# Kernel optimization log

Hardware: AMD Instinct MI355X
Metric: run time of the kernel (lower is better)

The kernel has to match this reference:

```python
import jax, jax.numpy as jnp
import numpy as np

N = 50_000
E = 800_000
H = 128
EDGE_DIM = 1
NEG = 0.01  # leaky_relu slope used throughout AttentiveFP


def _lrelu(x):
    return jnp.where(x >= 0, x, NEG * x)


def _seg_softmax(logits, seg, num_segments):
    # numerically stable softmax over edges grouped by target segment
    m = jax.ops.segment_max(logits, seg, num_segments=num_segments)
    e = jnp.exp(logits - m[seg])
    s = jax.ops.segment_sum(e, seg, num_segments=num_segments)
    return e / s[seg]


def _gru(x, h, Wih, Whh, bih, bhh):
    # torch.nn.GRUCell: gates ordered r, z, n
    gi = x @ Wih.T + bih
    gh = h @ Whh.T + bhh
    ir, iz, inn = jnp.split(gi, 3, axis=-1)
    hr, hz, hn = jnp.split(gh, 3, axis=-1)
    r = jax.nn.sigmoid(ir + hr)
    z = jax.nn.sigmoid(iz + hz)
    n = jnp.tanh(inn + r * hn)
    return (1.0 - z) * n + z * h


def setup_inputs() -> dict:
    key = jax.random.key(0)
    ks = jax.random.split(key, 32)
    def rn(k, shape, s=0.1):
        return jax.random.normal(k, shape, dtype=jnp.float32) * s
    return {
        "node_attr": jax.random.normal(ks[0], (N, 1), dtype=jnp.float32),
        "edge_index": jax.random.randint(ks[1], (2, E), 0, N),
        "edge_attr": jax.random.normal(ks[2], (E, EDGE_DIM), dtype=jnp.float32),
        "W_lin1": rn(ks[3], (H, 1)), "b_lin1": rn(ks[4], (H,)),
        "gate_W1": rn(ks[5], (H, H + EDGE_DIM)), "gate_W2": rn(ks[6], (H, H)),
        "gate_att_l": rn(ks[7], (H,)), "gate_att_r": rn(ks[8], (H,)),
        "gate_b": rn(ks[9], (H,)),
        "gru1_Wih": rn(ks[10], (3 * H, H)), "gru1_Whh": rn(ks[11], (3 * H, H)),
        "gru1_bih": rn(ks[12], (3 * H,)), "gru1_bhh": rn(ks[13], (3 * H,)),
        "atom_W": rn(ks[14], (H, H)), "atom_att_src": rn(ks[15], (H,)),
        "atom_att_dst": rn(ks[16], (H,)), "atom_b": rn(ks[17], (H,)),
        "gru2_Wih": rn(ks[18], (3 * H, H)), "gru2_Whh": rn(ks[19], (3 * H, H)),
        "gru2_bih": rn(ks[20], (3 * H,)), "gru2_bhh": rn(ks[21], (3 * H,)),
        "mol_W": rn(ks[22], (H, H)), "mol_att_src": rn(ks[23], (H,)),
        "mol_att_dst": rn(ks[24], (H,)), "mol_b": rn(ks[25], (H,)),
        "grum_Wih": rn(ks[26], (3 * H, H)), "grum_Whh": rn(ks[27], (3 * H, H)),
        "grum_bih": rn(ks[28], (3 * H,)), "grum_bhh": rn(ks[29], (3 * H,)),
    }


def _forward(node_attr, edge_index, edge_attr, W_lin1, b_lin1, gate_W1, gate_W2,
             gate_att_l, gate_att_r, gate_b, gru1_Wih, gru1_Whh, gru1_bih, gru1_bhh,
             atom_W, atom_att_src, atom_att_dst, atom_b, gru2_Wih, gru2_Whh,
             gru2_bih, gru2_bhh, mol_W, mol_att_src, mol_att_dst, mol_b,
             grum_Wih, grum_Whh, grum_bih, grum_bhh):
    src, dst = edge_index[0], edge_index[1]  # j -> i (aggregate at dst)
    n = node_attr.shape[0]
    # lin1 + leaky_relu
    x = _lrelu(node_attr @ W_lin1.T + b_lin1)  # [N,H]
    # --- GATEConv (edge-featured attention) ---
    xj = _lrelu(jnp.concatenate([x[src], edge_attr], axis=-1) @ gate_W1.T)  # [E,H]
    alpha = _lrelu(xj @ gate_att_l + (x @ gate_att_r)[dst])  # [E]
    alpha = _seg_softmax(alpha, dst, n)
    h = jax.ops.segment_sum((x[src] @ gate_W2.T) * alpha[:, None], dst, num_segments=n) + gate_b
    h = jax.nn.elu(h)
    x = jax.nn.relu(_gru(h, x, gru1_Wih, gru1_Whh, gru1_bih, gru1_bhh))
    # --- GATConv layer (num_layers=2 -> one) ---
    xt = x @ atom_W.T  # [N,H]
    a = _lrelu((xt * atom_att_src).sum(-1)[src] + (xt * atom_att_dst).sum(-1)[dst])
    a = _seg_softmax(a, dst, n)
    h = jax.ops.segment_sum(xt[src] * a[:, None], dst, num_segments=n) + atom_b
    h = jax.nn.elu(h)
    x = jax.nn.relu(_gru(h, x, gru2_Wih, gru2_Whh, gru2_bih, gru2_bhh))
    # --- molecule embedding: batch = zeros -> single graph; num_timesteps=1 ---
    batch = jnp.zeros((n,), dtype=jnp.int32)
    out = jax.nn.relu(jax.ops.segment_sum(x, batch, num_segments=1))  # [1,H]
    xs = x @ mol_W.T          # node-side transform (shared lin)
    outs = out @ mol_W.T      # graph-side transform
    a = _lrelu((xs * mol_att_src).sum(-1) + (outs * mol_att_dst).sum(-1)[batch])
    a = _seg_softmax(a, batch, 1)
    h = jax.nn.elu(jax.ops.segment_sum(xs * a[:, None], batch, num_segments=1) + mol_b)
    out = jax.nn.relu(_gru(h, out, grum_Wih, grum_Whh, grum_bih, grum_bhh))
    return out  # [1, H] graph embedding (layer1 output, out_channels=hidden)


def reference(node_attr, edge_index, edge_attr, W_lin1, b_lin1, gate_W1, gate_W2,
              gate_att_l, gate_att_r, gate_b, gru1_Wih, gru1_Whh, gru1_bih, gru1_bhh,
              atom_W, atom_att_src, atom_att_dst, atom_b, gru2_Wih, gru2_Whh,
              gru2_bih, gru2_bhh, mol_W, mol_att_src, mol_att_dst, mol_b,
              grum_Wih, grum_Whh, grum_bih, grum_bhh):
    return _forward(node_attr, edge_index, edge_attr, W_lin1, b_lin1, gate_W1,
                    gate_W2, gate_att_l, gate_att_r, gate_b, gru1_Wih, gru1_Whh,
                    gru1_bih, gru1_bhh, atom_W, atom_att_src, atom_att_dst, atom_b,
                    gru2_Wih, gru2_Whh, gru2_bih, gru2_bhh, mol_W, mol_att_src,
                    mol_att_dst, mol_b, grum_Wih, grum_Whh, grum_bih, grum_bhh)
```

## Files before the change

kernel.cpp:

```cpp
#include <hip/hip_runtime.h>
#include <math.h>

#define H 128
#define NEGS 0.01f

typedef __attribute__((ext_vector_type(8))) short short8;
typedef __attribute__((ext_vector_type(4))) float f32x4;

__device__ __forceinline__ float lrelu(float x){ return x >= 0.f ? x : NEGS*x; }
__device__ __forceinline__ float eluf(float x){ return x > 0.f ? x : expf(x)-1.f; }
__device__ __forceinline__ float sigm(float x){ return 1.f/(1.f+expf(-x)); }
__device__ __forceinline__ float wred(float v){
  #pragma unroll
  for (int off = 32; off > 0; off >>= 1) v += __shfl_xor(v, off, 64);
  return v;
}
__device__ __forceinline__ float wredmax(float v){
  #pragma unroll
  for (int off = 32; off > 0; off >>= 1) v = fmaxf(v, __shfl_xor(v, off, 64));
  return v;
}
__device__ __forceinline__ unsigned fenc(float f){
  unsigned u = __float_as_uint(f);
  return (u & 0x80000000u) ? ~u : (u | 0x80000000u);
}
__device__ __forceinline__ float fdec(unsigned v){
  return __uint_as_float((v & 0x80000000u) ? (v ^ 0x80000000u) : ~v);
}
__device__ __forceinline__ unsigned short f2bf(float f){
  unsigned u = __float_as_uint(f);
  u += 0x7fffu + ((u >> 16) & 1u);
  return (unsigned short)(u >> 16);
}
__device__ __forceinline__ float bf2f(unsigned short h){
  return __uint_as_float(((unsigned)h) << 16);
}
__device__ __forceinline__ float rdlane(float v, int l){
  return __int_as_float(__builtin_amdgcn_readlane(__float_as_int(v), l));
}
__device__ __forceinline__ int rdlanei(int v, int l){
  return __builtin_amdgcn_readlane(v, l);
}

__global__ void k_castall(const float* __restrict__ gW1, const float* __restrict__ gW2,
                          const float* __restrict__ atomW, const float* __restrict__ molW,
                          const float* __restrict__ g1ih, const float* __restrict__ g1hh,
                          const float* __restrict__ g2ih, const float* __restrict__ g2hh,
                          unsigned short* __restrict__ dst){
  int idx = blockIdx.x*256 + threadIdx.x;
  const float* src; int ld = 128; int off;
  if      (idx <  16384){ src = gW1;  ld = 129; off = idx; }
  else if (idx <  32768){ src = gW2;  off = idx -  16384; }
  else if (idx <  49152){ src = atomW;off = idx -  32768; }
  else if (idx <  65536){ src = molW; off = idx -  49152; }
  else if (idx < 114688){ src = g1ih; off = idx -  65536; }
  else if (idx < 163840){ src = g1hh; off = idx - 114688; }
  else if (idx < 212992){ src = g2ih; off = idx - 163840; }
  else                  { src = g2hh; off = idx - 212992; }
  int r = off >> 7, c = off & 127;
  dst[idx] = f2bf(src[r*ld + c]);
}

__global__ void k_node_init_rd(const float* __restrict__ na, const float* __restrict__ wl,
                               const float* __restrict__ bl, const float* __restrict__ attr,
                               unsigned short* __restrict__ x, float* __restrict__ rdot, int n){
  int i = blockIdx.x*4 + (threadIdx.x >> 6);
  int lane = threadIdx.x & 63;
  if (i >= n) return;
  float nav = na[i];
  float v0 = lrelu(nav*wl[2*lane]   + bl[2*lane]);
  float v1 = lrelu(nav*wl[2*lane+1] + bl[2*lane+1]);
  ushort2 o; o.x = f2bf(v0); o.y = f2bf(v1);
  *(ushort2*)&x[(size_t)i*H + 2*lane] = o;
  float d = bf2f(o.x)*attr[2*lane] + bf2f(o.y)*attr[2*lane+1];
  d = wred(d);
  if (lane == 0) rdot[i] = d;
}

__global__ __launch_bounds__(256)
void k_gemm_mfma(const unsigned short* __restrict__ X, const unsigned short* __restrict__ Wbf,
                 unsigned short* __restrict__ Y, int n, int ldy,
                 const float* __restrict__ v1, const float* __restrict__ v2,
                 float* __restrict__ o1, float* __restrict__ o2){
  int w = threadIdx.x >> 6;
  int l = threadIdx.x & 63;
  int i0 = blockIdx.x*64 + w*16;
  int mbase = blockIdx.y*128;
  int row = l & 15;
  int kg  = l >> 4;
  f32x4 acc[8];
  #pragma unroll
  for (int c = 0; c < 8; ++c) acc[c] = (f32x4){0.f,0.f,0.f,0.f};
  int ai = i0 + row;
  bool av = (ai < n);
  #pragma unroll
  for (int ks = 0; ks < 4; ++ks){
    int koff = ks*32 + kg*8;
    short8 a = av ? *(const short8*)&X[(size_t)ai*H + koff]
                  : (short8){0,0,0,0,0,0,0,0};
    #pragma unroll
    for (int c = 0; c < 8; ++c){
      short8 b = *(const short8*)&Wbf[(size_t)(mbase + c*16 + row)*H + koff];
      acc[c] = __builtin_amdgcn_mfma_f32_16x16x32_bf16(a, b, acc[c], 0, 0, 0);
    }
  }
  #pragma unroll
  for (int c = 0; c < 8; ++c){
    #pragma unroll
    for (int r = 0; r < 4; ++r){
      int i = i0 + kg*4 + r;
      if (i < n) Y[(size_t)i*ldy + mbase + c*16 + row] = f2bf(acc[c][r]);
    }
  }
  if (v1){
    #pragma unroll
    for (int r = 0; r < 4; ++r){
      float p1 = 0.f, p2 = 0.f;
      #pragma unroll
      for (int c = 0; c < 8; ++c){
        float av1 = v1[c*16 + row];
        p1 += acc[c][r]*av1;
        if (v2) p2 += acc[c][r]*v2[c*16 + row];
      }
      #pragma unroll
      for (int off = 1; off < 16; off <<= 1){
        p1 += __shfl_xor(p1, off, 64);
        if (v2) p2 += __shfl_xor(p2, off, 64);
      }
      int i = i0 + kg*4 + r;
      if (row == 0 && i < n){ o1[i] = p1; if (v2) o2[i] = p2; }
    }
  }
}

__global__ void k_gru_combine(const unsigned short* __restrict__ gi, const unsigned short* __restrict__ gh,
                              const float* __restrict__ bih, const float* __restrict__ bhh,
                              unsigned short* __restrict__ x, int n){
  int idx = blockIdx.x*blockDim.x + threadIdx.x;
  if (idx >= n*64) return;
  int i = idx >> 6, t = (idx & 63)*2;
  const unsigned short* gir = gi + (size_t)i*384;
  const unsigned short* ghr = gh + (size_t)i*384;
  ushort2 uir = *(const ushort2*)&gir[t];
  ushort2 uiz = *(const ushort2*)&gir[t+128];
  ushort2 uin = *(const ushort2*)&gir[t+256];
  ushort2 uhr = *(const ushort2*)&ghr[t];
  ushort2 uhz = *(const ushort2*)&ghr[t+128];
  ushort2 uhn = *(const ushort2*)&ghr[t+256];
  ushort2 ux  = *(const ushort2*)&x[(size_t)i*H + t];
  float2 b_ir = *(const float2*)&bih[t], b_iz = *(const float2*)&bih[t+128], b_in = *(const float2*)&bih[t+256];
  float2 b_hr = *(const float2*)&bhh[t], b_hz = *(const float2*)&bhh[t+128], b_hn = *(const float2*)&bhh[t+256];
  ushort2 o;
  {
    float r = sigm(bf2f(uir.x)+b_ir.x + bf2f(uhr.x)+b_hr.x);
    float z = sigm(bf2f(uiz.x)+b_iz.x + bf2f(uhz.x)+b_hz.x);
    float nn = tanhf(bf2f(uin.x)+b_in.x + r*(bf2f(uhn.x)+b_hn.x));
    o.x = f2bf(fmaxf((1.f-z)*nn + z*bf2f(ux.x), 0.f));
  }
  {
    float r = sigm(bf2f(uir.y)+b_ir.y + bf2f(uhr.y)+b_hr.y);
    float z = sigm(bf2f(uiz.y)+b_iz.y + bf2f(uhz.y)+b_hz.y);
    float nn = tanhf(bf2f(uin.y)+b_in.y + r*(bf2f(uhn.y)+b_hn.y));
    o.y = f2bf(fmaxf((1.f-z)*nn + z*bf2f(ux.y), 0.f));
  }
  *(ushort2*)&x[(size_t)i*H + t] = o;
}

__global__ void k_hist(const int* __restrict__ dst, int* __restrict__ deg, int ne){
  int e = blockIdx.x*blockDim.x + threadIdx.x;
  if (e < ne) atomicAdd(&deg[dst[e]], 1);
}
__global__ void k_scan1(const int* __restrict__ deg, int* __restrict__ bsum, int n){
  __shared__ int sd[256];
  int i = blockIdx.x*256 + threadIdx.x;
  sd[threadIdx.x] = (i < n) ? deg[i] : 0;
  __syncthreads();
  for (int s = 128; s > 0; s >>= 1){
    if (threadIdx.x < s) sd[threadIdx.x] += sd[threadIdx.x+s];
    __syncthreads();
  }
  if (threadIdx.x == 0) bsum[blockIdx.x] = sd[0];
}
__global__ void k_scan2(int* __restrict__ bsum, int nb){
  __shared__ int sd[256];
  int t = threadIdx.x;
  int v = (t < nb) ? bsum[t] : 0;
  sd[t] = v;
  __syncthreads();
  for (int off = 1; off < 256; off <<= 1){
    int u = (t >= off) ? sd[t-off] : 0;
    __syncthreads();
    sd[t] += u;
    __syncthreads();
  }
  if (t < nb) bsum[t] = sd[t] - v;
}
__global__ void k_scan3(const int* __restrict__ deg, const int* __restrict__ boff,
                        int* __restrict__ rowptr, int* __restrict__ cursor, int n){
  __shared__ int sd[256];
  int t = threadIdx.x;
  int i = blockIdx.x*256 + t;
  int v = (i < n) ? deg[i] : 0;
  sd[t] = v;
  __syncthreads();
  for (int off = 1; off < 256; off <<= 1){
    int u = (t >= off) ? sd[t-off] : 0;
    __syncthreads();
    sd[t] += u;
    __syncthreads();
  }
  int excl = sd[t] - v + boff[blockIdx.x];
  if (i < n){
    rowptr[i] = excl; cursor[i] = excl;
    if (i == n-1) rowptr[n] = excl + v;
  }
}
__global__ void k_fill(const int* __restrict__ dst, int* __restrict__ cursor,
                       int* __restrict__ eid, int ne){
  int e = blockIdx.x*blockDim.x + threadIdx.x;
  if (e >= ne) return;
  int pos = atomicAdd(&cursor[dst[e]], 1);
  eid[pos] = e;
}

__global__ void k_pack_gate(const float* __restrict__ gateW1, float* __restrict__ w1col){
  int t = threadIdx.x;
  if (t < H) w1col[t] = gateW1[t*129 + 128];
}

__global__ __launch_bounds__(256)
void k_edge_logit_gate(const unsigned short* __restrict__ xW1, const float* __restrict__ w1col,
                       const float* __restrict__ attl, const float* __restrict__ rdot,
                       const float* __restrict__ ea, const int* __restrict__ src,
                       const int* __restrict__ dst, float* __restrict__ logit, int ne){
  int tid = threadIdx.x;
  int e = blockIdx.x*32 + (tid >> 3);
  int g = tid & 7;
  if (e >= ne) return;
  int s = src[e];
  float eav = ea[e];
  const unsigned short* xr = &xW1[(size_t)s*H + g*16];
  short8 r0 = *(const short8*)xr;
  short8 r1 = *(const short8*)(xr + 8);
  float acc = 0.f;
  #pragma unroll
  for (int k = 0; k < 8; ++k)
    acc += lrelu(bf2f((unsigned short)r0[k]) + eav*w1col[g*16 + k]) * attl[g*16 + k];
  #pragma unroll
  for (int k = 0; k < 8; ++k)
    acc += lrelu(bf2f((unsigned short)r1[k]) + eav*w1col[g*16 + 8 + k]) * attl[g*16 + 8 + k];
  #pragma unroll
  for (int off = 1; off < 8; off <<= 1) acc += __shfl_xor(acc, off, 64);
  if (g == 0) logit[e] = lrelu(acc + rdot[dst[e]]);
}

__global__ void k_node_agg(const int* __restrict__ rowptr, const int* __restrict__ eid,
                           const int* __restrict__ src, const float* __restrict__ logit,
                           const unsigned short* __restrict__ val, const float* __restrict__ bias,
                           unsigned short* __restrict__ hbuf, int n){
  int i = blockIdx.x*4 + (threadIdx.x >> 6);
  int lane = threadIdx.x & 63;
  if (i >= n) return;
  int b = rowptr[i], e1 = rowptr[i+1];
  float m = -1e30f;
  for (int j = b+lane; j < e1; j += 64) m = fmaxf(m, logit[eid[j]]);
  m = wredmax(m);
  float s = 0.f, ax = 0.f, ay = 0.f;
  for (int c0 = b; c0 < e1; c0 += 64){
    int cnt = min(64, e1 - c0);
    float wv = 0.f; int snv = 0;
    if (lane < cnt){
      int e = eid[c0 + lane];
      snv = src[e];
      wv = expf(logit[e] - m);
    }
    s += wred(wv);
    int j = 0;
    for (; j+8 <= cnt; j += 8){
      #pragma unroll
      for (int u = 0; u < 8; ++u){
        float wq = rdlane(wv, j+u);
        int sq = rdlanei(snv, j+u);
        ushort2 v = *(const ushort2*)&val[(size_t)sq*H + 2*lane];
        ax += bf2f(v.x)*wq; ay += bf2f(v.y)*wq;
      }
    }
    for (; j < cnt; ++j){
      float wq = rdlane(wv, j);
      int sq = rdlanei(snv, j);
      ushort2 v = *(const ushort2*)&val[(size_t)sq*H + 2*lane];
      ax += bf2f(v.x)*wq; ay += bf2f(v.y)*wq;
    }
  }
  float inv = (s > 0.f) ? 1.f/s : 0.f;
  ushort2 o;
  o.x = f2bf(eluf(bias[2*lane]   + ax*inv));
  o.y = f2bf(eluf(bias[2*lane+1] + ay*inv));
  *(ushort2*)&hbuf[(size_t)i*H + 2*lane] = o;
}

__global__ void k_node_agg_gat(const int* __restrict__ rowptr, const int* __restrict__ eid,
                               const int* __restrict__ src, const float* __restrict__ ssrc,
                               const float* __restrict__ sdst, const unsigned short* __restrict__ val,
                               const float* __restrict__ bias, unsigned short* __restrict__ hbuf, int n){
  int i = blockIdx.x*4 + (threadIdx.x >> 6);
  int lane = threadIdx.x & 63;
  if (i >= n) return;
  int b = rowptr[i], e1 = rowptr[i+1];
  float sdi = sdst[i];
  float m = -1e30f;
  for (int j = b+lane; j < e1; j += 64) m = fmaxf(m, lrelu(ssrc[src[eid[j]]] + sdi));
  m = wredmax(m);
  float s = 0.f, ax = 0.f, ay = 0.f;
  for (int c0 = b; c0 < e1; c0 += 64){
    int cnt = min(64, e1 - c0);
    float wv = 0.f; int snv = 0;
    if (lane < cnt){
      snv = src[eid[c0 + lane]];
      wv = expf(lrelu(ssrc[snv] + sdi) - m);
    }
    s += wred(wv);
    int j = 0;
    for (; j+8 <= cnt; j += 8){
      #pragma unroll
      for (int u = 0; u < 8; ++u){
        float wq = rdlane(wv, j+u);
        int sq = rdlanei(snv, j+u);
        ushort2 v = *(const ushort2*)&val[(size_t)sq*H + 2*lane];
        ax += bf2f(v.x)*wq; ay += bf2f(v.y)*wq;
      }
    }
    for (; j < cnt; ++j){
      float wq = rdlane(wv, j);
      int sq = rdlanei(snv, j);
      ushort2 v = *(const ushort2*)&val[(size_t)sq*H + 2*lane];
      ax += bf2f(v.x)*wq; ay += bf2f(v.y)*wq;
    }
  }
  float inv = (s > 0.f) ? 1.f/s : 0.f;
  ushort2 o;
  o.x = f2bf(eluf(bias[2*lane]   + ax*inv));
  o.y = f2bf(eluf(bias[2*lane+1] + ay*inv));
  *(ushort2*)&hbuf[(size_t)i*H + 2*lane] = o;
}

__global__ void k_colsum(const unsigned short* __restrict__ x, float* __restrict__ outraw,
                         int n, int chunk){
  int t = threadIdx.x;
  int start = blockIdx.x*chunk;
  int end = min(start + chunk, n);
  float s0 = 0.f, s1 = 0.f;
  for (int i = start; i < end; ++i){
    ushort2 v = *(const ushort2*)&x[(size_t)i*H + 2*t];
    s0 += bf2f(v.x); s1 += bf2f(v.y);
  }
  if (start < end){ atomicAdd(&outraw[2*t], s0); atomicAdd(&outraw[2*t+1], s1); }
}
__global__ void k_mol_prep(const float* __restrict__ outraw, const float* __restrict__ molW,
                           const float* __restrict__ attdst, float* __restrict__ hidvec,
                           float* __restrict__ cdst){
  __shared__ float hs[128];
  __shared__ float red[128];
  int t = threadIdx.x;
  float hv = fmaxf(outraw[t], 0.f);
  hs[t] = hv; hidvec[t] = hv;
  __syncthreads();
  float o = 0.f;
  for (int k = 0; k < 128; ++k) o += hs[k]*molW[t*128+k];
  red[t] = o * attdst[t];
  __syncthreads();
  for (int s = 64; s > 0; s >>= 1){
    if (t < s) red[t] += red[t+s];
    __syncthreads();
  }
  if (t == 0) cdst[0] = red[0];
}
__global__ void k_mol_logit(float* __restrict__ a, const float* __restrict__ cdst,
                            unsigned* __restrict__ gmax, int n){
  int i = blockIdx.x*blockDim.x + threadIdx.x;
  if (i >= n) return;
  float l = lrelu(a[i] + cdst[0]);
  a[i] = l;
  atomicMax(gmax, fenc(l));
}
__global__ void k_mol_exp(float* __restrict__ a, const unsigned* __restrict__ gmax,
                          float* __restrict__ gsum, int n){
  int i = blockIdx.x*blockDim.x + threadIdx.x;
  int lane = threadIdx.x & 63;
  float gm = fdec(gmax[0]);
  float ex = 0.f;
  if (i < n){ ex = expf(a[i] - gm); a[i] = ex; }
  float s = wred(ex);
  if (lane == 0) atomicAdd(gsum, s);
}
__global__ void k_mol_acc(const unsigned short* __restrict__ xs, const float* __restrict__ a,
                          float* __restrict__ num, int n, int chunk){
  int t = threadIdx.x;
  int start = blockIdx.x*chunk;
  int end = min(start + chunk, n);
  float s0 = 0.f, s1 = 0.f;
  for (int i = start; i < end; ++i){
    float ai = a[i];
    ushort2 v = *(const ushort2*)&xs[(size_t)i*H + 2*t];
    s0 += bf2f(v.x)*ai; s1 += bf2f(v.y)*ai;
  }
  if (start < end){ atomicAdd(&num[2*t], s0); atomicAdd(&num[2*t+1], s1); }
}
__global__ void k_mol_final(const float* __restrict__ num, const float* __restrict__ gsum,
                            const float* __restrict__ molb, const float* __restrict__ hidvec,
                            const float* __restrict__ Wih, const float* __restrict__ Whh,
                            const float* __restrict__ bih, const float* __restrict__ bhh,
                            float* __restrict__ out){
  __shared__ float hv[128], hd[128];
  int t = threadIdx.x;
  hv[t] = eluf(num[t]/gsum[0] + molb[t]);
  hd[t] = hidvec[t];
  __syncthreads();
  float gr = bih[t], gz = bih[t+128], gn = bih[t+256];
  float hr = bhh[t], hz = bhh[t+128], hn = bhh[t+256];
  for (int k = 0; k < 128; ++k){
    float h = hv[k], d = hd[k];
    gr += h*Wih[t*128+k];       gz += h*Wih[(t+128)*128+k]; gn += h*Wih[(t+256)*128+k];
    hr += d*Whh[t*128+k];       hz += d*Whh[(t+128)*128+k]; hn += d*Whh[(t+256)*128+k];
  }
  float r = sigm(gr+hr), z = sigm(gz+hz);
  float nn = tanhf(gn + r*hn);
  float o = (1.f-z)*nn + z*hd[t];
  out[t] = fmaxf(o, 0.f);
}

extern "C" void kernel_launch(void* const* d_in, const int* in_sizes, int n_in,
                              void* d_out, int out_size, void* d_ws, size_t ws_size,
                              hipStream_t stream){
  const float* node_attr = (const float*)d_in[0];
  const int*   eidx      = (const int*)d_in[1];
  const float* eattr     = (const float*)d_in[2];
  const float* W_lin1    = (const float*)d_in[3];
  const float* b_lin1    = (const float*)d_in[4];
  const float* gate_W1   = (const float*)d_in[5];
  const float* gate_W2   = (const float*)d_in[6];
  const float* gate_att_l= (const float*)d_in[7];
  const float* gate_att_r= (const float*)d_in[8];
  const float* gate_b    = (const float*)d_in[9];
  const float* g1_Wih    = (const float*)d_in[10];
  const float* g1_Whh    = (const float*)d_in[11];
  const float* g1_bih    = (const float*)d_in[12];
  const float* g1_bhh    = (const float*)d_in[13];
  const float* atom_W    = (const float*)d_in[14];
  const float* atom_as   = (const float*)d_in[15];
  const float* atom_ad   = (const float*)d_in[16];
  const float* atom_b    = (const float*)d_in[17];
  const float* g2_Wih    = (const float*)d_in[18];
  const float* g2_Whh    = (const float*)d_in[19];
  const float* g2_bih    = (const float*)d_in[20];
  const float* g2_bhh    = (const float*)d_in[21];
  const float* mol_W     = (const float*)d_in[22];
  const float* mol_as    = (const float*)d_in[23];
  const float* mol_ad    = (const float*)d_in[24];
  const float* mol_b     = (const float*)d_in[25];
  const float* gm_Wih    = (const float*)d_in[26];
  const float* gm_Whh    = (const float*)d_in[27];
  const float* gm_bih    = (const float*)d_in[28];
  const float* gm_bhh    = (const float*)d_in[29];

  const int n  = in_sizes[0];
  const int ne = in_sizes[1] / 2;
  const int* src = eidx;
  const int* dst = eidx + ne;

  const size_t NH = (size_t)n * H;
  unsigned short* us = (unsigned short*)d_ws;
  unsigned short* x_bf = us;
  unsigned short* t0   = us + NH;
  unsigned short* t1   = us + 2*NH;
  unsigned short* hb   = us + 3*NH;
  unsigned short* gi   = us + 4*NH;
  unsigned short* gh   = us + 7*NH;
  float* fb = (float*)(us + 10*NH);
  float* rdot = fb;
  float* ssrc = rdot + n;
  float* sdst = ssrc + n;
  float* ealpha = sdst + n;
  int* deg    = (int*)(ealpha + ne);
  int* cursor = deg + n;
  int* rowptr = cursor + n;
  int* bsum   = rowptr + n + 1;
  int* eid    = bsum + 256;
  float* outraw = (float*)(eid + ne);
  float* hidvec = outraw + 128;
  float* cdstp  = hidvec + 128;
  unsigned* gmax = (unsigned*)(cdstp + 1);
  float* gsum   = (float*)gmax + 1;
  float* numv   = gsum + 1;
  float* w1col  = numv + 128;
  unsigned short* wp = (unsigned short*)(w1col + 128);
  unsigned short* gW1bf  = wp;
  unsigned short* gW2bf  = gW1bf  + 128*H;
  unsigned short* atomWbf= gW2bf  + 128*H;
  unsigned short* molWbf = atomWbf+ 128*H;
  unsigned short* g1ihbf = molWbf + 128*H;
  unsigned short* g1hhbf = g1ihbf + 384*H;
  unsigned short* g2ihbf = g1hhbf + 384*H;
  unsigned short* g2hhbf = g2ihbf + 384*H;

  const int nb64       = (n + 63)/64;
  const int nwave4     = (n + 3)/4;
  const int e32_blocks = (ne + 31)/32;
  const int ethr       = (ne + 255)/256;
  const int nthr       = (n + 255)/256;
  const int nb         = (n + 255)/256;
  const int chunk      = (n + 255)/256;
  const int gru_blocks = (n*64 + 255)/256;

  k_castall<<<1024,256,0,stream>>>(gate_W1, gate_W2, atom_W, mol_W,
                                   g1_Wih, g1_Whh, g2_Wih, g2_Whh, wp);
  k_pack_gate<<<1,128,0,stream>>>(gate_W1, w1col);
  k_node_init_rd<<<nwave4,256,0,stream>>>(node_attr, W_lin1, b_lin1, gate_att_r, x_bf, rdot, n);
  hipMemsetAsync(deg, 0, (size_t)n*4, stream);
  k_hist<<<ethr,256,0,stream>>>(dst, deg, ne);
  k_scan1<<<nb,256,0,stream>>>(deg, bsum, n);
  k_scan2<<<1,256,0,stream>>>(bsum, nb);
  k_scan3<<<nb,256,0,stream>>>(deg, bsum, rowptr, cursor, n);
  k_fill<<<ethr,256,0,stream>>>(dst, cursor, eid, ne);

  k_gemm_mfma<<<dim3(nb64,1),256,0,stream>>>(x_bf, gW1bf, t0, n, H,
                                             nullptr, nullptr, nullptr, nullptr);
  k_gemm_mfma<<<dim3(nb64,1),256,0,stream>>>(x_bf, gW2bf, t1, n, H,
                                             nullptr, nullptr, nullptr, nullptr);
  k_edge_logit_gate<<<e32_blocks,256,0,stream>>>(t0, w1col, gate_att_l, rdot, eattr,
                                                 src, dst, ealpha, ne);
  k_node_agg<<<nwave4,256,0,stream>>>(rowptr, eid, src, ealpha, t1, gate_b, hb, n);
  k_gemm_mfma<<<dim3(nb64,3),256,0,stream>>>(hb,   g1ihbf, gi, n, 384,
                                             nullptr, nullptr, nullptr, nullptr);
  k_gemm_mfma<<<dim3(nb64,3),256,0,stream>>>(x_bf, g1hhbf, gh, n, 384,
                                             nullptr, nullptr, nullptr, nullptr);
  k_gru_combine<<<gru_blocks,256,0,stream>>>(gi, gh, g1_bih, g1_bhh, x_bf, n);

  k_gemm_mfma<<<dim3(nb64,1),256,0,stream>>>(x_bf, atomWbf, t0, n, H,
                                             atom_as, atom_ad, ssrc, sdst);
  k_node_agg_gat<<<nwave4,256,0,stream>>>(rowptr, eid, src, ssrc, sdst, t0, atom_b, hb, n);
  k_gemm_mfma<<<dim3(nb64,3),256,0,stream>>>(hb,   g2ihbf, gi, n, 384,
                                             nullptr, nullptr, nullptr, nullptr);
  k_gemm_mfma<<<dim3(nb64,3),256,0,stream>>>(x_bf, g2hhbf, gh, n, 384,
                                             nullptr, nullptr, nullptr, nullptr);
  k_gru_combine<<<gru_blocks,256,0,stream>>>(gi, gh, g2_bih, g2_bhh, x_bf, n);

  hipMemsetAsync(outraw, 0, 128*4, stream);
  hipMemsetAsync(gmax, 0, 4, stream);
  hipMemsetAsync(gsum, 0, 4, stream);
  hipMemsetAsync(numv, 0, 128*4, stream);
  k_colsum<<<256,64,0,stream>>>(x_bf, outraw, n, chunk);
  k_mol_prep<<<1,128,0,stream>>>(outraw, mol_W, mol_ad, hidvec, cdstp);
  k_gemm_mfma<<<dim3(nb64,1),256,0,stream>>>(x_bf, molWbf, t1, n, H,
                                             mol_as, nullptr, rdot, nullptr);
  k_mol_logit<<<nthr,256,0,stream>>>(rdot, cdstp, gmax, n);
  k_mol_exp<<<nthr,256,0,stream>>>(rdot, gmax, gsum, n);
  k_mol_acc<<<256,64,0,stream>>>(t1, rdot, numv, n, chunk);
  k_mol_final<<<1,128,0,stream>>>(numv, gsum, mol_b, hidvec,
                                  gm_Wih, gm_Whh, gm_bih, gm_bhh, (float*)d_out);
}
```

Measured before the change: 741.4 us.

## Store CSR-sorted source ids and src-sort edges for gate logit locality

The edge-to-node CSR fill now writes source ids in destination-sorted order, so the two aggregation kernels read src_s contiguously instead of going through an eid indirection. A second CSR, sorted by source, drives the gate logit kernel so consecutive edges share cached xW1 rows. Raw logits are written in CSR position and the dst term plus leaky_relu are applied inside aggregation. The molecular logit max now reduces within each wave before doing one atomic per wave, at the cost of an extra histogram, scan and fill pass over the edges.

```diff
diff --git a/kernel.cpp b/kernel.cpp
--- a/kernel.cpp
+++ b/kernel.cpp
@@ -118,8 +118,7 @@
       float p1 = 0.f, p2 = 0.f;
       #pragma unroll
       for (int c = 0; c < 8; ++c){
-        float av1 = v1[c*16 + row];
-        p1 += acc[c][r]*av1;
+        p1 += acc[c][r]*v1[c*16 + row];
         if (v2) p2 += acc[c][r]*v2[c*16 + row];
       }
       #pragma unroll
@@ -166,9 +165,9 @@
   *(ushort2*)&x[(size_t)i*H + t] = o;
 }
 
-__global__ void k_hist(const int* __restrict__ dst, int* __restrict__ deg, int ne){
+__global__ void k_hist(const int* __restrict__ key, int* __restrict__ deg, int ne){
   int e = blockIdx.x*blockDim.x + threadIdx.x;
-  if (e < ne) atomicAdd(&deg[dst[e]], 1);
+  if (e < ne) atomicAdd(&deg[key[e]], 1);
 }
 __global__ void k_scan1(const int* __restrict__ deg, int* __restrict__ bsum, int n){
   __shared__ int sd[256];
@@ -215,12 +214,22 @@
     if (i == n-1) rowptr[n] = excl + v;
   }
 }
-__global__ void k_fill(const int* __restrict__ dst, int* __restrict__ cursor,
-                       int* __restrict__ eid, int ne){
+__global__ void k_fill_dst(const int* __restrict__ src, const int* __restrict__ dst,
+                           const float* __restrict__ ea, int* __restrict__ cursor,
+                           int* __restrict__ src_s, int2* __restrict__ posea, int ne){
   int e = blockIdx.x*blockDim.x + threadIdx.x;
   if (e >= ne) return;
   int pos = atomicAdd(&cursor[dst[e]], 1);
-  eid[pos] = e;
+  src_s[pos] = src[e];
+  posea[e] = make_int2(pos, __float_as_int(ea[e]));
+}
+__global__ void k_fill_src(const int* __restrict__ src, int* __restrict__ cursor2,
+                           int* __restrict__ eperm, int* __restrict__ sperm, int ne){
+  int e = blockIdx.x*blockDim.x + threadIdx.x;
+  if (e >= ne) return;
+  int s = src[e];
+  int p = atomicAdd(&cursor2[s], 1);
+  eperm[p] = e; sperm[p] = s;
 }
 
 __global__ void k_pack_gate(const float* __restrict__ gateW1, float* __restrict__ w1col){
@@ -230,49 +239,51 @@
 
 __global__ __launch_bounds__(256)
 void k_edge_logit_gate(const unsigned short* __restrict__ xW1, const float* __restrict__ w1col,
-                       const float* __restrict__ attl, const float* __restrict__ rdot,
-                       const float* __restrict__ ea, const int* __restrict__ src,
-                       const int* __restrict__ dst, float* __restrict__ logit, int ne){
+                       const float* __restrict__ attl, const int* __restrict__ eperm,
+                       const int* __restrict__ sperm, const int2* __restrict__ posea,
+                       float* __restrict__ logit_s, int ne){
   int tid = threadIdx.x;
-  int e = blockIdx.x*32 + (tid >> 3);
+  int k = blockIdx.x*32 + (tid >> 3);
   int g = tid & 7;
-  if (e >= ne) return;
-  int s = src[e];
-  float eav = ea[e];
+  if (k >= ne) return;
+  int e = eperm[k];
+  int s = sperm[k];
+  int2 pe = posea[e];
+  float eav = __int_as_float(pe.y);
   const unsigned short* xr = &xW1[(size_t)s*H + g*16];
   short8 r0 = *(const short8*)xr;
   short8 r1 = *(const short8*)(xr + 8);
   float acc = 0.f;
   #pragma unroll
-  for (int k = 0; k < 8; ++k)
-    acc += lrelu(bf2f((unsigned short)r0[k]) + eav*w1col[g*16 + k]) * attl[g*16 + k];
-  #pragma unroll
-  for (int k = 0; k < 8; ++k)
-    acc += lrelu(bf2f((unsigned short)r1[k]) + eav*w1col[g*16 + 8 + k]) * attl[g*16 + 8 + k];
+  for (int kk = 0; kk < 8; ++kk)
+    acc += lrelu(bf2f((unsigned short)r0[kk]) + eav*w1col[g*16 + kk]) * attl[g*16 + kk];
+  #pragma unroll
+  for (int kk = 0; kk < 8; ++kk)
+    acc += lrelu(bf2f((unsigned short)r1[kk]) + eav*w1col[g*16 + 8 + kk]) * attl[g*16 + 8 + kk];
   #pragma unroll
   for (int off = 1; off < 8; off <<= 1) acc += __shfl_xor(acc, off, 64);
-  if (g == 0) logit[e] = lrelu(acc + rdot[dst[e]]);
-}
-
-__global__ void k_node_agg(const int* __restrict__ rowptr, const int* __restrict__ eid,
-                           const int* __restrict__ src, const float* __restrict__ logit,
+  if (g == 0) logit_s[pe.x] = acc;
+}
+
+__global__ void k_node_agg(const int* __restrict__ rowptr, const int* __restrict__ src_s,
+                           const float* __restrict__ logit_s, const float* __restrict__ rdot,
                            const unsigned short* __restrict__ val, const float* __restrict__ bias,
                            unsigned short* __restrict__ hbuf, int n){
   int i = blockIdx.x*4 + (threadIdx.x >> 6);
   int lane = threadIdx.x & 63;
   if (i >= n) return;
   int b = rowptr[i], e1 = rowptr[i+1];
+  float rd = rdot[i];
   float m = -1e30f;
-  for (int j = b+lane; j < e1; j += 64) m = fmaxf(m, logit[eid[j]]);
+  for (int j = b+lane; j < e1; j += 64) m = fmaxf(m, lrelu(logit_s[j] + rd));
   m = wredmax(m);
   float s = 0.f, ax = 0.f, ay = 0.f;
   for (int c0 = b; c0 < e1; c0 += 64){
     int cnt = min(64, e1 - c0);
     float wv = 0.f; int snv = 0;
     if (lane < cnt){
-      int e = eid[c0 + lane];
-      snv = src[e];
-      wv = expf(logit[e] - m);
+      snv = src_s[c0 + lane];
+      wv = expf(lrelu(logit_s[c0 + lane] + rd) - m);
     }
     s += wred(wv);
     int j = 0;
@@ -299,24 +310,24 @@
   *(ushort2*)&hbuf[(size_t)i*H + 2*lane] = o;
 }
 
-__global__ void k_node_agg_gat(const int* __restrict__ rowptr, const int* __restrict__ eid,
-                               const int* __restrict__ src, const float* __restrict__ ssrc,
-                               const float* __restrict__ sdst, const unsigned short* __restrict__ val,
-                               const float* __restrict__ bias, unsigned short* __restrict__ hbuf, int n){
+__global__ void k_node_agg_gat(const int* __restrict__ rowptr, const int* __restrict__ src_s,
+                               const float* __restrict__ ssrc, const float* __restrict__ sdst,
+                               const unsigned short* __restrict__ val, const float* __restrict__ bias,
+                               unsigned short* __restrict__ hbuf, int n){
   int i = blockIdx.x*4 + (threadIdx.x >> 6);
   int lane = threadIdx.x & 63;
   if (i >= n) return;
   int b = rowptr[i], e1 = rowptr[i+1];
   float sdi = sdst[i];
   float m = -1e30f;
-  for (int j = b+lane; j < e1; j += 64) m = fmaxf(m, lrelu(ssrc[src[eid[j]]] + sdi));
+  for (int j = b+lane; j < e1; j += 64) m = fmaxf(m, lrelu(ssrc[src_s[j]] + sdi));
   m = wredmax(m);
   float s = 0.f, ax = 0.f, ay = 0.f;
   for (int c0 = b; c0 < e1; c0 += 64){
     int cnt = min(64, e1 - c0);
     float wv = 0.f; int snv = 0;
     if (lane < cnt){
-      snv = src[eid[c0 + lane]];
+      snv = src_s[c0 + lane];
       wv = expf(lrelu(ssrc[snv] + sdi) - m);
     }
     s += wred(wv);
@@ -378,10 +389,14 @@
 __global__ void k_mol_logit(float* __restrict__ a, const float* __restrict__ cdst,
                             unsigned* __restrict__ gmax, int n){
   int i = blockIdx.x*blockDim.x + threadIdx.x;
-  if (i >= n) return;
-  float l = lrelu(a[i] + cdst[0]);
-  a[i] = l;
-  atomicMax(gmax, fenc(l));
+  int lane = threadIdx.x & 63;
+  float l = -1e30f;
+  if (i < n){
+    l = lrelu(a[i] + cdst[0]);
+    a[i] = l;
+  }
+  float mm = wredmax(l);
+  if (lane == 0) atomicMax(gmax, fenc(mm));
 }
 __global__ void k_mol_exp(float* __restrict__ a, const unsigned* __restrict__ gmax,
                           float* __restrict__ gsum, int n){
@@ -480,19 +495,28 @@
   float* rdot = fb;
   float* ssrc = rdot + n;
   float* sdst = ssrc + n;
-  float* ealpha = sdst + n;
-  int* deg    = (int*)(ealpha + ne);
+  float* logit_s = sdst + n;
+  int* deg    = (int*)(logit_s + ne);
   int* cursor = deg + n;
   int* rowptr = cursor + n;
   int* bsum   = rowptr + n + 1;
-  int* eid    = bsum + 256;
-  float* outraw = (float*)(eid + ne);
+  int* deg2   = bsum + 256;
+  int* cursor2= deg2 + n;
+  int* rowptr2= cursor2 + n;
+  int* bsum2  = rowptr2 + n + 1;
+  int* src_s  = bsum2 + 256;
+  int* eperm  = src_s + ne;
+  int* sperm  = eperm + ne;
+  size_t ioff = (size_t)(sperm + ne - (int*)d_ws);
+  ioff = (ioff + 1) & ~(size_t)1;
+  int2* posea = (int2*)((int*)d_ws + ioff);
+  float* outraw = (float*)(posea + ne);
   float* hidvec = outraw + 128;
   float* cdstp  = hidvec + 128;
   unsigned* gmax = (unsigned*)(cdstp + 1);
   float* gsum   = (float*)gmax + 1;
   float* numv   = gsum + 1;
-  float* w1col  = numv + 128;
+  float* w1col  = numv + 128 + 1;
   unsigned short* wp = (unsigned short*)(w1col + 128);
   unsigned short* gW1bf  = wp;
   unsigned short* gW2bf  = gW1bf  + 128*H;
@@ -517,19 +541,25 @@
   k_pack_gate<<<1,128,0,stream>>>(gate_W1, w1col);
   k_node_init_rd<<<nwave4,256,0,stream>>>(node_attr, W_lin1, b_lin1, gate_att_r, x_bf, rdot, n);
   hipMemsetAsync(deg, 0, (size_t)n*4, stream);
+  hipMemsetAsync(deg2, 0, (size_t)n*4, stream);
   k_hist<<<ethr,256,0,stream>>>(dst, deg, ne);
   k_scan1<<<nb,256,0,stream>>>(deg, bsum, n);
   k_scan2<<<1,256,0,stream>>>(bsum, nb);
   k_scan3<<<nb,256,0,stream>>>(deg, bsum, rowptr, cursor, n);
-  k_fill<<<ethr,256,0,stream>>>(dst, cursor, eid, ne);
+  k_fill_dst<<<ethr,256,0,stream>>>(src, dst, eattr, cursor, src_s, posea, ne);
+  k_hist<<<ethr,256,0,stream>>>(src, deg2, ne);
+  k_scan1<<<nb,256,0,stream>>>(deg2, bsum2, n);
+  k_scan2<<<1,256,0,stream>>>(bsum2, nb);
+  k_scan3<<<nb,256,0,stream>>>(deg2, bsum2, rowptr2, cursor2, n);
+  k_fill_src<<<ethr,256,0,stream>>>(src, cursor2, eperm, sperm, ne);
 
   k_gemm_mfma<<<dim3(nb64,1),256,0,stream>>>(x_bf, gW1bf, t0, n, H,
                                              nullptr, nullptr, nullptr, nullptr);
   k_gemm_mfma<<<dim3(nb64,1),256,0,stream>>>(x_bf, gW2bf, t1, n, H,
                                              nullptr, nullptr, nullptr, nullptr);
-  k_edge_logit_gate<<<e32_blocks,256,0,stream>>>(t0, w1col, gate_att_l, rdot, eattr,
-                                                 src, dst, ealpha, ne);
-  k_node_agg<<<nwave4,256,0,stream>>>(rowptr, eid, src, ealpha, t1, gate_b, hb, n);
+  k_edge_logit_gate<<<e32_blocks,256,0,stream>>>(t0, w1col, gate_att_l,
+                                                 eperm, sperm, posea, logit_s, ne);
+  k_node_agg<<<nwave4,256,0,stream>>>(rowptr, src_s, logit_s, rdot, t1, gate_b, hb, n);
   k_gemm_mfma<<<dim3(nb64,3),256,0,stream>>>(hb,   g1ihbf, gi, n, 384,
                                              nullptr, nullptr, nullptr, nullptr);
   k_gemm_mfma<<<dim3(nb64,3),256,0,stream>>>(x_bf, g1hhbf, gh, n, 384,
@@ -538,7 +568,7 @@
 
   k_gemm_mfma<<<dim3(nb64,1),256,0,stream>>>(x_bf, atomWbf, t0, n, H,
                                              atom_as, atom_ad, ssrc, sdst);
-  k_node_agg_gat<<<nwave4,256,0,stream>>>(rowptr, eid, src, ssrc, sdst, t0, atom_b, hb, n);
+  k_node_agg_gat<<<nwave4,256,0,stream>>>(rowptr, src_s, ssrc, sdst, t0, atom_b, hb, n);
   k_gemm_mfma<<<dim3(nb64,3),256,0,stream>>>(hb,   g2ihbf, gi, n, 384,
                                              nullptr, nullptr, nullptr, nullptr);
   k_gemm_mfma<<<dim3(nb64,3),256,0,stream>>>(x_bf, g2hhbf, gh, n, 384,
```

Measured after the change: 834.4 us. 1.13x slower.
